# Optimization experiments

Hardware: AMD Instinct MI355X
Metric: run time of the kernel (lower is better)

## Reference

```python
import jax, jax.numpy as jnp
import numpy as np

N, C, H, W = 64, 64, 8, 8        # batch, img_net_out_dim, feature-map spatial dims
E = 256                           # ques_rnn_hidden_dim
G = 256                           # rn_g_dim
F_DIM = 256                       # rn_f_dim
NUM_CLASSES = 2
D = C + 2                         # per-object feature dim (channels + 2 loc coords)
G_IN = 2 * D + E                  # 388


def setup_inputs() -> dict:
    key = jax.random.key(0)
    ks = jax.random.split(key, 10)

    def w(k, shape):
        fan_in = shape[0]
        return jax.random.normal(k, shape, dtype=jnp.float32) / np.sqrt(fan_in).astype(np.float32)

    return {
        "img": jax.random.normal(ks[0], (N, C, H, W), dtype=jnp.float32),
        "ques": jax.random.normal(ks[1], (N, E), dtype=jnp.float32),
        "g_w1": w(ks[2], (G_IN, G)), "g_b1": jnp.zeros((G,), jnp.float32),
        "g_w2": w(ks[3], (G, G)),    "g_b2": jnp.zeros((G,), jnp.float32),
        "g_w3": w(ks[4], (G, G)),    "g_b3": jnp.zeros((G,), jnp.float32),
        "g_w4": w(ks[5], (G, G)),    "g_b4": jnp.zeros((G,), jnp.float32),
        "f_w1": w(ks[6], (G, F_DIM)),       "f_b1": jnp.zeros((F_DIM,), jnp.float32),
        "f_w2": w(ks[7], (F_DIM, F_DIM)),   "f_b2": jnp.zeros((F_DIM,), jnp.float32),
        "f_w3": w(ks[8], (F_DIM, NUM_CLASSES)), "f_b3": jnp.zeros((NUM_CLASSES,), jnp.float32),
    }


def _img_to_pairs(img, ques):
    # img: (N, C, H, W); ques: (N, E) -> pairs: (N, O*O, 2*(C+2)+E)
    n, c, h, w = img.shape
    o = h * w
    cells = img.reshape(n, c, o)
    idx = jnp.arange(o)
    loc = jnp.stack([idx // w, idx % w], axis=0).astype(img.dtype)      # (2, O)
    cells = jnp.concatenate([cells, jnp.broadcast_to(loc, (n, 2, o))], axis=1)  # (N, D, O)
    cells = cells.transpose(0, 2, 1)                                    # (N, O, D)
    d = cells.shape[-1]
    one = jnp.broadcast_to(cells[:, :, None, :], (n, o, o, d))          # object i
    two = jnp.broadcast_to(cells[:, None, :, :], (n, o, o, d))          # object j
    three = jnp.broadcast_to(ques[:, None, None, :], (n, o, o, ques.shape[-1]))
    pairs = jnp.concatenate([one, two, three], axis=-1)                 # (N, O, O, G_IN)
    return pairs.reshape(n, o * o, -1)


def reference(img, ques, g_w1, g_b1, g_w2, g_b2, g_w3, g_b3, g_w4, g_b4,
              f_w1, f_b1, f_w2, f_b2, f_w3, f_b3):
    n = img.shape[0]
    pairs = _img_to_pairs(img, ques)                  # (N, P, G_IN)
    x = pairs.reshape(-1, pairs.shape[-1])            # (N*P, G_IN)
    x = jax.nn.relu(x @ g_w1 + g_b1)
    x = jax.nn.relu(x @ g_w2 + g_b2)
    x = jax.nn.relu(x @ g_w3 + g_b3)
    x = jax.nn.relu(x @ g_w4 + g_b4)
    context = x.reshape(n, -1, x.shape[-1]).mean(axis=1)   # (N, G)
    # f MLP: Linear+ReLU, Linear+ReLU, Dropout(eval=identity), Linear
    y = jax.nn.relu(context @ f_w1 + f_b1)
    y = jax.nn.relu(y @ f_w2 + f_b2)
    scores = y @ f_w3 + f_b3                          # (N, 2)
    return jax.nn.log_softmax(scores, axis=1)
```

## Files before the change

kernel.cpp:

```cpp
#include <hip/hip_runtime.h>
#include <hip/hip_bf16.h>

typedef __bf16 bf16x8 __attribute__((ext_vector_type(8)));
typedef __bf16 bf16x4 __attribute__((ext_vector_type(4)));
typedef float  f32x4  __attribute__((ext_vector_type(4)));

__global__ __launch_bounds__(256) void prep_kernel(
    const float* __restrict__ img, const float* __restrict__ ques,
    const float* __restrict__ g_w1, const float* __restrict__ g_b1,
    const float* __restrict__ g_w2, const float* __restrict__ g_w3,
    const float* __restrict__ g_w4,
    float* __restrict__ U, float* __restrict__ V, float* __restrict__ Qb,
    __bf16* __restrict__ W2t, __bf16* __restrict__ W3t, __bf16* __restrict__ W4t) {
  __shared__ float smem[64 * 65];
  const int blk = blockIdx.x;
  const int t = threadIdx.x;

  if (blk < 512) {
    const int n = blk >> 3, obase = (blk & 7) * 8;
    for (int idx = t; idx < 66 * 8; idx += 256) {
      const int c = idx >> 3, o = obase + (idx & 7);
      float v;
      if (c < 64)      v = img[n * 4096 + c * 64 + o];
      else if (c == 64) v = (float)(o >> 3);
      else              v = (float)(o & 7);
      smem[idx] = v;
    }
    __syncthreads();
    float u[8], vv[8];
#pragma unroll
    for (int o = 0; o < 8; ++o) { u[o] = 0.f; vv[o] = 0.f; }
#pragma unroll 2
    for (int d = 0; d < 66; ++d) {
      const float wu = g_w1[d * 256 + t];
      const float wv = g_w1[(66 + d) * 256 + t];
#pragma unroll
      for (int o = 0; o < 8; ++o) {
        const float cc = smem[d * 8 + o];
        u[o]  += cc * wu;
        vv[o] += cc * wv;
      }
    }
#pragma unroll
    for (int o = 0; o < 8; ++o) {
      U[(size_t)(n * 64 + obase + o) * 256 + t] = u[o];
      V[(size_t)(n * 64 + obase + o) * 256 + t] = vv[o];
    }
  } else if (blk < 576) {
    const int n = blk - 512;
    smem[t] = ques[n * 256 + t];
    __syncthreads();
    float s = g_b1[t];
    for (int e = 0; e < 256; ++e) s += smem[e] * g_w1[(132 + e) * 256 + t];
    Qb[n * 256 + t] = s;
  } else {
    const int b2 = blk - 576;
    const int wsel = b2 >> 4;
    const int tile = b2 & 15;
    const int r0 = (tile >> 2) * 64, c0 = (tile & 3) * 64;
    const float* W = (wsel == 0) ? g_w2 : (wsel == 1) ? g_w3 : g_w4;
    __bf16* Wt    = (wsel == 0) ? W2t  : (wsel == 1) ? W3t  : W4t;
    const int col = t & 63, rb = (t >> 6) * 16;
#pragma unroll 4
    for (int j = 0; j < 16; ++j)
      smem[(rb + j) * 65 + col] = W[(size_t)(r0 + rb + j) * 256 + c0 + col];
    __syncthreads();
#pragma unroll 4
    for (int j = 0; j < 16; ++j)
      Wt[(size_t)(c0 + rb + j) * 256 + r0 + col] = (__bf16)smem[col * 65 + rb + j];
  }
}

#define CH 520

template <bool LAST>
__device__ __forceinline__ void g_layer(__bf16* Hs,
                                        bf16x8 bb[2][2],
                                        const __bf16* __restrict__ Wcur,
                                        const __bf16* __restrict__ Wnext,
                                        int woff, int lane8, int wb,
                                        const float* __restrict__ bias_g,
                                        int nq, int q, int r16,
                                        float* __restrict__ pr0,
                                        float* __restrict__ pr1) {
  f32x4 acc[8][2];
  {
    const f32x4 bv0 = *(const f32x4*)&bias_g[nq * 32 + 0 * 16 + q * 4];
    const f32x4 bv1 = *(const f32x4*)&bias_g[nq * 32 + 1 * 16 + q * 4];
#pragma unroll
    for (int m = 0; m < 8; ++m) {
      acc[m][0] = bv0;
      acc[m][1] = bv1;
    }
  }

#pragma unroll
  for (int ks = 0; ks < 8; ++ks) {
    const bf16x8 b0 = bb[ks & 1][0];
    const bf16x8 b1 = bb[ks & 1][1];
    if (ks < 7) {
      bb[(ks + 1) & 1][0] = *(const bf16x8*)&Wcur[woff + (ks + 1) * 32];
      bb[(ks + 1) & 1][1] = *(const bf16x8*)&Wcur[woff + 4096 + (ks + 1) * 32];
    } else if (!LAST) {
      bb[0][0] = *(const bf16x8*)&Wnext[woff];
      bb[0][1] = *(const bf16x8*)&Wnext[woff + 4096];
    }
#pragma unroll
    for (int m = 0; m < 8; ++m) {
      const bf16x8 a = *(const bf16x8*)&Hs[(m * 8 + ks) * CH + lane8];
      acc[m][0] = __builtin_amdgcn_mfma_f32_16x16x32_bf16(b0, a, acc[m][0], 0, 0, 0);
      acc[m][1] = __builtin_amdgcn_mfma_f32_16x16x32_bf16(b1, a, acc[m][1], 0, 0, 0);
    }
  }

  if (!LAST) {
    __syncthreads();
#pragma unroll
    for (int m = 0; m < 8; ++m)
#pragma unroll
      for (int nt = 0; nt < 2; ++nt) {
        bf16x4 h;
#pragma unroll
        for (int r = 0; r < 4; ++r) h[r] = (__bf16)fmaxf(acc[m][nt][r], 0.f);
        *(bf16x4*)&Hs[wb + m * (8 * CH) + nt * 256] = h;
      }
    __syncthreads();
  } else {
#pragma unroll
    for (int h = 0; h < 2; ++h) {
#pragma unroll
      for (int nt = 0; nt < 2; ++nt) {
        const int cb = nq * 32 + nt * 16 + q * 4;
        f32x4 s;
#pragma unroll
        for (int r = 0; r < 4; ++r)
          s[r] = fmaxf(acc[h * 4 + 0][nt][r], 0.f)
               + fmaxf(acc[h * 4 + 1][nt][r], 0.f)
               + fmaxf(acc[h * 4 + 2][nt][r], 0.f)
               + fmaxf(acc[h * 4 + 3][nt][r], 0.f);
#pragma unroll
        for (int d = 1; d < 16; d <<= 1) {
#pragma unroll
          for (int r = 0; r < 4; ++r) s[r] += __shfl_xor(s[r], d, 64);
        }
        if (r16 == 0) *(f32x4*)&(h ? pr1 : pr0)[cb] = s;
      }
    }
  }
}

__global__ __launch_bounds__(512, 4) void rn_main(
    const float* __restrict__ U, const float* __restrict__ V,
    const float* __restrict__ Qb,
    const __bf16* __restrict__ W2t, const __bf16* __restrict__ W3t,
    const __bf16* __restrict__ W4t,
    const float* __restrict__ b2, const float* __restrict__ b3,
    const float* __restrict__ b4,
    float* __restrict__ part) {
  __shared__ __align__(16) __bf16 Hs[64 * CH];
  const int blk = blockIdx.x;
  const int nimg = blk >> 5, ipair = blk & 31;
  const int iobj0 = ipair * 2;
  const int t = threadIdx.x;
  const int nq = t >> 6, lane = t & 63;
  const int q = lane >> 4, r16 = lane & 15;

  const int woff = (nq * 32 + r16) * 256 + q * 8;
  const int lane8 = lane * 8;
  const int wb = nq * CH + (q >> 1) * 128 + r16 * 8 + (q & 1) * 4;

  bf16x8 bb[2][2];
  bb[0][0] = *(const bf16x8*)&W2t[woff];
  bb[0][1] = *(const bf16x8*)&W2t[woff + 4096];

  {
    const int c4 = t & 63;
    const int rb = t >> 6;
    const int isel = rb >> 2;
    const int pb = (rb * 8 + (c4 >> 3)) * CH + ((c4 >> 1) & 3) * 128 + (c4 & 1) * 4;
    const f32x4 u4 = *(const f32x4*)&U[(size_t)(nimg * 64 + iobj0 + isel) * 256 + c4 * 4];
    const f32x4 q4 = *(const f32x4*)&Qb[(size_t)nimg * 256 + c4 * 4];
    const f32x4 uq = u4 + q4;
#pragma unroll
    for (int jj = 0; jj < 16; ++jj) {
      const int j = (rb & 3) * 16 + jj;
      const f32x4 v4 = *(const f32x4*)&V[(size_t)(nimg * 64 + j) * 256 + c4 * 4];
      bf16x4 h;
#pragma unroll
      for (int r = 0; r < 4; ++r) h[r] = (__bf16)fmaxf(uq[r] + v4[r], 0.f);
      *(bf16x4*)&Hs[pb + jj * 8] = h;
    }
  }
  __syncthreads();

  float* pr0 = part + (size_t)blk * 512;
  float* pr1 = pr0 + 256;

  g_layer<false>(Hs, bb, W2t, W3t, woff, lane8, wb, b2, nq, q, r16, pr0, pr1);
  g_layer<false>(Hs, bb, W3t, W4t, woff, lane8, wb, b3, nq, q, r16, pr0, pr1);
  g_layer<true >(Hs, bb, W4t, W4t, woff, lane8, wb, b4, nq, q, r16, pr0, pr1);
}

__global__ __launch_bounds__(1024) void rn_final(
    const float* __restrict__ part,
    const float* __restrict__ f_w1, const float* __restrict__ f_b1,
    const float* __restrict__ f_w2, const float* __restrict__ f_b2,
    const float* __restrict__ f_w3, const float* __restrict__ f_b3,
    float* __restrict__ out) {
  __shared__ float red[4][256];
  __shared__ float ctx[256], y1[256], y2[256], sc[2];
  const int n = blockIdx.x;
  const int tid = threadIdx.x;
  const int o = tid & 255, g = tid >> 8;

  {
    float s = 0.f;
#pragma unroll 4
    for (int i = 0; i < 16; ++i)
      s += part[((size_t)n * 64 + g * 16 + i) * 256 + o];
    red[g][o] = s;
  }
  __syncthreads();
  if (g == 0)
    ctx[o] = (red[0][o] + red[1][o] + red[2][o] + red[3][o]) * (1.0f / 4096.0f);
  __syncthreads();

  {
    float a = 0.f;
#pragma unroll 4
    for (int k = 0; k < 64; ++k)
      a += ctx[g * 64 + k] * f_w1[(g * 64 + k) * 256 + o];
    red[g][o] = a;
  }
  __syncthreads();
  if (g == 0)
    y1[o] = fmaxf(red[0][o] + red[1][o] + red[2][o] + red[3][o] + f_b1[o], 0.f);
  __syncthreads();

  {
    float a = 0.f;
#pragma unroll 4
    for (int k = 0; k < 64; ++k)
      a += y1[g * 64 + k] * f_w2[(g * 64 + k) * 256 + o];
    red[g][o] = a;
  }
  __syncthreads();
  if (g == 0)
    y2[o] = fmaxf(red[0][o] + red[1][o] + red[2][o] + red[3][o] + f_b2[o], 0.f);
  __syncthreads();

  if (tid < 2) {
    float c = f_b3[tid];
    for (int k = 0; k < 256; ++k) c += y2[k] * f_w3[k * 2 + tid];
    sc[tid] = c;
  }
  __syncthreads();
  if (tid == 0) {
    const float s0 = sc[0], s1 = sc[1];
    const float mx = fmaxf(s0, s1);
    const float lse = mx + logf(expf(s0 - mx) + expf(s1 - mx));
    out[n * 2 + 0] = s0 - lse;
    out[n * 2 + 1] = s1 - lse;
  }
}

extern "C" void kernel_launch(void* const* d_in, const int* in_sizes, int n_in,
                              void* d_out, int out_size, void* d_ws, size_t ws_size,
                              hipStream_t stream) {
  const float* img  = (const float*)d_in[0];
  const float* ques = (const float*)d_in[1];
  const float* g_w1 = (const float*)d_in[2];
  const float* g_b1 = (const float*)d_in[3];
  const float* g_w2 = (const float*)d_in[4];
  const float* g_b2 = (const float*)d_in[5];
  const float* g_w3 = (const float*)d_in[6];
  const float* g_b3 = (const float*)d_in[7];
  const float* g_w4 = (const float*)d_in[8];
  const float* g_b4 = (const float*)d_in[9];
  const float* f_w1 = (const float*)d_in[10];
  const float* f_b1 = (const float*)d_in[11];
  const float* f_w2 = (const float*)d_in[12];
  const float* f_b2 = (const float*)d_in[13];
  const float* f_w3 = (const float*)d_in[14];
  const float* f_b3 = (const float*)d_in[15];
  float* out = (float*)d_out;

  char* ws = (char*)d_ws;
  float*  U    = (float*)(ws);
  float*  V    = (float*)(ws + (size_t)4  * 1048576);
  float*  part = (float*)(ws + (size_t)8  * 1048576);
  float*  Qb   = (float*)(ws + (size_t)12 * 1048576);
  __bf16* W2t  = (__bf16*)(ws + (size_t)12 * 1048576 + 65536);
  __bf16* W3t  = W2t + 65536;
  __bf16* W4t  = W3t + 65536;

  prep_kernel<<<624, 256, 0, stream>>>(img, ques, g_w1, g_b1, g_w2, g_w3, g_w4,
                                       U, V, Qb, W2t, W3t, W4t);
  rn_main<<<2048, 512, 0, stream>>>(U, V, Qb, W2t, W3t, W4t, g_b2, g_b3, g_b4, part);
  rn_final<<<64, 1024, 0, stream>>>(part, f_w1, f_b1, f_w2, f_b2, f_w3, f_b3, out);
}
```

Baseline: 224.1 us.

## Switch g-MLP layers from 16x16x32 to 32x32x16 MFMA with 2D wave tiling

```diff
diff --git a/kernel.cpp b/kernel.cpp
--- a/kernel.cpp
+++ b/kernel.cpp
@@ -4,6 +4,7 @@
 typedef __bf16 bf16x8 __attribute__((ext_vector_type(8)));
 typedef __bf16 bf16x4 __attribute__((ext_vector_type(4)));
 typedef float  f32x4  __attribute__((ext_vector_type(4)));
+typedef float  f32x16 __attribute__((ext_vector_type(16)));
 
 __global__ __launch_bounds__(256) void prep_kernel(
     const float* __restrict__ img, const float* __restrict__ ques,
@@ -78,72 +79,81 @@
                                         bf16x8 bb[2][2],
                                         const __bf16* __restrict__ Wcur,
                                         const __bf16* __restrict__ Wnext,
-                                        int woff, int lane8, int wb,
+                                        int woff, int rbase, int wchunk,
+                                        int wlane, int cbb,
                                         const float* __restrict__ bias_g,
-                                        int nq, int q, int r16,
+                                        int rw, int l31,
                                         float* __restrict__ pr0,
                                         float* __restrict__ pr1) {
-  f32x4 acc[8][2];
-  {
-    const f32x4 bv0 = *(const f32x4*)&bias_g[nq * 32 + 0 * 16 + q * 4];
-    const f32x4 bv1 = *(const f32x4*)&bias_g[nq * 32 + 1 * 16 + q * 4];
-#pragma unroll
-    for (int m = 0; m < 8; ++m) {
-      acc[m][0] = bv0;
-      acc[m][1] = bv1;
-    }
-  }
-
-#pragma unroll
-  for (int ks = 0; ks < 8; ++ks) {
+  f32x16 acc[2][2];
+#pragma unroll
+  for (int nt = 0; nt < 2; ++nt)
+#pragma unroll
+    for (int rg = 0; rg < 4; ++rg) {
+      const f32x4 bv = *(const f32x4*)&bias_g[cbb + nt * 32 + rg * 8];
+#pragma unroll
+      for (int j = 0; j < 4; ++j) {
+        acc[0][nt][rg * 4 + j] = bv[j];
+        acc[1][nt][rg * 4 + j] = bv[j];
+      }
+    }
+
+#pragma unroll
+  for (int ks = 0; ks < 16; ++ks) {
     const bf16x8 b0 = bb[ks & 1][0];
     const bf16x8 b1 = bb[ks & 1][1];
-    if (ks < 7) {
-      bb[(ks + 1) & 1][0] = *(const bf16x8*)&Wcur[woff + (ks + 1) * 32];
-      bb[(ks + 1) & 1][1] = *(const bf16x8*)&Wcur[woff + 4096 + (ks + 1) * 32];
+    if (ks < 15) {
+      bb[(ks + 1) & 1][0] = *(const bf16x8*)&Wcur[woff + (ks + 1) * 16];
+      bb[(ks + 1) & 1][1] = *(const bf16x8*)&Wcur[woff + 8192 + (ks + 1) * 16];
     } else if (!LAST) {
       bb[0][0] = *(const bf16x8*)&Wnext[woff];
-      bb[0][1] = *(const bf16x8*)&Wnext[woff + 4096];
-    }
-#pragma unroll
-    for (int m = 0; m < 8; ++m) {
-      const bf16x8 a = *(const bf16x8*)&Hs[(m * 8 + ks) * CH + lane8];
-      acc[m][0] = __builtin_amdgcn_mfma_f32_16x16x32_bf16(b0, a, acc[m][0], 0, 0, 0);
-      acc[m][1] = __builtin_amdgcn_mfma_f32_16x16x32_bf16(b1, a, acc[m][1], 0, 0, 0);
-    }
+      bb[0][1] = *(const bf16x8*)&Wnext[woff + 8192];
+    }
+    const bf16x8 a0 = *(const bf16x8*)&Hs[rbase + ks * CH];
+    const bf16x8 a1 = *(const bf16x8*)&Hs[rbase + (16 + ks) * CH];
+    acc[0][0] = __builtin_amdgcn_mfma_f32_32x32x16_bf16(b0, a0, acc[0][0], 0, 0, 0);
+    acc[0][1] = __builtin_amdgcn_mfma_f32_32x32x16_bf16(b1, a0, acc[0][1], 0, 0, 0);
+    acc[1][0] = __builtin_amdgcn_mfma_f32_32x32x16_bf16(b0, a1, acc[1][0], 0, 0, 0);
+    acc[1][1] = __builtin_amdgcn_mfma_f32_32x32x16_bf16(b1, a1, acc[1][1], 0, 0, 0);
   }
 
   if (!LAST) {
     __syncthreads();
 #pragma unroll
-    for (int m = 0; m < 8; ++m)
-#pragma unroll
-      for (int nt = 0; nt < 2; ++nt) {
-        bf16x4 h;
-#pragma unroll
-        for (int r = 0; r < 4; ++r) h[r] = (__bf16)fmaxf(acc[m][nt][r], 0.f);
-        *(bf16x4*)&Hs[wb + m * (8 * CH) + nt * 256] = h;
+    for (int m = 0; m < 2; ++m)
+#pragma unroll
+      for (int nt = 0; nt < 2; ++nt)
+#pragma unroll
+        for (int rg = 0; rg < 4; ++rg) {
+          bf16x4 h;
+#pragma unroll
+          for (int j = 0; j < 4; ++j)
+            h[j] = (__bf16)fmaxf(acc[m][nt][rg * 4 + j], 0.f);
+          *(bf16x4*)&Hs[wchunk + (m * 16 + nt * 2 + (rg >> 1)) * CH
+                        + wlane + (rg & 1) * 256] = h;
+        }
+    __syncthreads();
+  } else {
+    float* pr = rw ? pr1 : pr0;
+#pragma unroll
+    for (int nt = 0; nt < 2; ++nt) {
+      float s[16];
+#pragma unroll
+      for (int e = 0; e < 16; ++e)
+        s[e] = fmaxf(acc[0][nt][e], 0.f) + fmaxf(acc[1][nt][e], 0.f);
+#pragma unroll
+      for (int d = 1; d <= 16; d <<= 1) {
+#pragma unroll
+        for (int e = 0; e < 16; ++e) s[e] += __shfl_xor(s[e], d, 64);
       }
-    __syncthreads();
-  } else {
-#pragma unroll
-    for (int h = 0; h < 2; ++h) {
-#pragma unroll
-      for (int nt = 0; nt < 2; ++nt) {
-        const int cb = nq * 32 + nt * 16 + q * 4;
-        f32x4 s;
-#pragma unroll
-        for (int r = 0; r < 4; ++r)
-          s[r] = fmaxf(acc[h * 4 + 0][nt][r], 0.f)
-               + fmaxf(acc[h * 4 + 1][nt][r], 0.f)
-               + fmaxf(acc[h * 4 + 2][nt][r], 0.f)
-               + fmaxf(acc[h * 4 + 3][nt][r], 0.f);
-#pragma unroll
-        for (int d = 1; d < 16; d <<= 1) {
-#pragma unroll
-          for (int r = 0; r < 4; ++r) s[r] += __shfl_xor(s[r], d, 64);
+      if (l31 == 0) {
+#pragma unroll
+        for (int rg = 0; rg < 4; ++rg) {
+          f32x4 v;
+          v[0] = s[rg * 4 + 0]; v[1] = s[rg * 4 + 1];
+          v[2] = s[rg * 4 + 2]; v[3] = s[rg * 4 + 3];
+          *(f32x4*)&pr[cbb + nt * 32 + rg * 8] = v;
         }
-        if (r16 == 0) *(f32x4*)&(h ? pr1 : pr0)[cb] = s;
       }
     }
   }
@@ -163,21 +173,25 @@
   const int iobj0 = ipair * 2;
   const int t = threadIdx.x;
   const int nq = t >> 6, lane = t & 63;
-  const int q = lane >> 4, r16 = lane & 15;
-
-  const int woff = (nq * 32 + r16) * 256 + q * 8;
-  const int lane8 = lane * 8;
-  const int wb = nq * CH + (q >> 1) * 128 + r16 * 8 + (q & 1) * 4;
+  const int rw = nq >> 2, cw = nq & 3;
+  const int l31 = lane & 31, lhi = lane >> 5;
+
+  const int woff = (cw * 64 + l31) * 256 + lhi * 8;
+  const int rbase  = rw * 32 * CH + lane * 8;
+  const int wchunk = (rw * 32 + cw * 4) * CH;
+  const int wlane  = l31 * 8 + lhi * 4;
+  const int cbb    = cw * 64 + lhi * 4;
 
   bf16x8 bb[2][2];
   bb[0][0] = *(const bf16x8*)&W2t[woff];
-  bb[0][1] = *(const bf16x8*)&W2t[woff + 4096];
+  bb[0][1] = *(const bf16x8*)&W2t[woff + 8192];
 
   {
     const int c4 = t & 63;
     const int rb = t >> 6;
     const int isel = rb >> 2;
-    const int pb = (rb * 8 + (c4 >> 3)) * CH + ((c4 >> 1) & 3) * 128 + (c4 & 1) * 4;
+    const int pb = ((rb >> 1) * 16 + (c4 >> 2)) * CH
+                 + (((c4 >> 1) & 1) * 32 + (rb & 1) * 16) * 8 + (c4 & 1) * 4;
     const f32x4 u4 = *(const f32x4*)&U[(size_t)(nimg * 64 + iobj0 + isel) * 256 + c4 * 4];
     const f32x4 q4 = *(const f32x4*)&Qb[(size_t)nimg * 256 + c4 * 4];
     const f32x4 uq = u4 + q4;
@@ -196,9 +210,9 @@
   float* pr0 = part + (size_t)blk * 512;
   float* pr1 = pr0 + 256;
 
-  g_layer<false>(Hs, bb, W2t, W3t, woff, lane8, wb, b2, nq, q, r16, pr0, pr1);
-  g_layer<false>(Hs, bb, W3t, W4t, woff, lane8, wb, b3, nq, q, r16, pr0, pr1);
-  g_layer<true >(Hs, bb, W4t, W4t, woff, lane8, wb, b4, nq, q, r16, pr0, pr1);
+  g_layer<false>(Hs, bb, W2t, W3t, woff, rbase, wchunk, wlane, cbb, b2, rw, l31, pr0, pr1);
+  g_layer<false>(Hs, bb, W3t, W4t, woff, rbase, wchunk, wlane, cbb, b3, rw, l31, pr0, pr1);
+  g_layer<true >(Hs, bb, W4t, W4t, woff, rbase, wchunk, wlane, cbb, b4, rw, l31, pr0, pr1);
 }
 
 __global__ __launch_bounds__(1024) void rn_final(
```

New measurement: 326.0 us. 45.5% more time.
